# Optimization experiments

Measured on AMD Instinct MI355X. Metric: run time of the kernel, lower is better.

The kernel has to match this reference:

```python
import jax, jax.numpy as jnp
import numpy as np

N_NODES = 50000
N_EDGES = 800000
BASIS = 64
HIDDEN_RO = 128
N_GRAPHS = 512
T = 3


def setup_inputs() -> dict:
    key = jax.random.key(0)
    ks = jax.random.split(key, 12)
    Z = jax.random.randint(ks[0], (N_NODES,), 0, 10)
    edge_index = jax.random.randint(ks[1], (2, N_EDGES), 0, N_NODES)
    edge_attr = jax.random.normal(ks[2], (N_EDGES, BASIS), dtype=jnp.float32)
    batch = jnp.sort(jax.random.randint(ks[3], (N_NODES,), 0, N_GRAPHS))
    s = 1.0 / np.sqrt(BASIS)
    embed = jax.random.normal(ks[4], (10, BASIS), dtype=jnp.float32)
    cfW = jax.random.uniform(ks[5], (BASIS, BASIS), jnp.float32, -s, s)
    cfb = jax.random.uniform(ks[6], (BASIS,), jnp.float32, -s, s)
    dfW = jax.random.uniform(ks[7], (BASIS, BASIS), jnp.float32, -s, s)
    dfb = jax.random.uniform(ks[8], (BASIS,), jnp.float32, -s, s)
    fcW = jax.random.uniform(ks[9], (BASIS, BASIS), jnp.float32, -s, s)  # no bias
    W1 = jax.random.uniform(ks[10], (BASIS, HIDDEN_RO), jnp.float32, -s, s)
    b1 = jnp.zeros((HIDDEN_RO,), jnp.float32)
    W2 = jax.random.uniform(ks[11], (HIDDEN_RO, 4), jnp.float32, -1.0 / np.sqrt(HIDDEN_RO), 1.0 / np.sqrt(HIDDEN_RO))
    b2 = jnp.zeros((4,), jnp.float32)
    return {"Z": Z, "edge_index": edge_index, "edge_attr": edge_attr, "batch": batch,
            "embed": embed, "cfW": cfW, "cfb": cfb, "dfW": dfW, "dfb": dfb, "fcW": fcW,
            "W1": W1, "b1": b1, "W2": W2, "b2": b2}


def reference(Z, edge_index, edge_attr, batch, embed, cfW, cfb, dfW, dfb, fcW, W1, b1, W2, b2):
    src, dst = edge_index[0], edge_index[1]  # x_j gathered from src, aggregated at dst
    C = embed[Z]  # [N, basis]
    # df(edge_attr) does not depend on C; compute once (same math, shared weights)
    d_feat = edge_attr @ dfW + dfb  # [E, basis]
    for _ in range(T):
        c_feat = C[src] @ cfW + cfb            # gather + linear  [E, basis]
        msg = jnp.tanh((c_feat * d_feat) @ fcW)  # [E, basis]
        agg = jax.ops.segment_sum(msg, dst, num_segments=N_NODES)
        C = C + agg
    h = jnp.tanh(C @ W1 + b1) @ W2 + b2        # readout MLP [N, 4]
    return jax.ops.segment_sum(h, batch, num_segments=N_GRAPHS)  # global_add_pool [G, 4]
```

## Files before the change

kernel.cpp:

```cpp
#include <hip/hip_runtime.h>
#include <math.h>

#define N_NODES   50000
#define N_EDGES   800000
#define BASIS     64
#define HIDDEN_RO 128
#define N_GRAPHS  512
#define T_ITERS   3
#define NB_SCAN   ((N_NODES + 255) / 256)

typedef short s8 __attribute__((ext_vector_type(8)));
typedef float f4 __attribute__((ext_vector_type(4)));

#define MFMA16(a, b, c) __builtin_amdgcn_mfma_f32_16x16x32_bf16(a, b, c, 0, 0, 0)

__device__ __forceinline__ float fast_tanh(float x) {
    float e = __expf(2.0f * x);
    return 1.0f - 2.0f / (e + 1.0f);
}

__device__ __forceinline__ f4 splat4(float x) { f4 v; v[0]=x; v[1]=x; v[2]=x; v[3]=x; return v; }

__device__ __forceinline__ void split8(const float* x, s8& hi, s8& lo) {
    union { unsigned a[4]; s8 v; } H, L;
    #pragma unroll
    for (int j = 0; j < 4; ++j) {
        float e0 = x[2*j], e1 = x[2*j+1];
        unsigned u0 = __float_as_uint(e0), u1 = __float_as_uint(e1);
        H.a[j] = (u0 >> 16) | (u1 & 0xFFFF0000u);
        float l0 = e0 - __uint_as_float(u0 & 0xFFFF0000u);
        float l1 = e1 - __uint_as_float(u1 & 0xFFFF0000u);
        L.a[j] = (__float_as_uint(l0) >> 16) | (__float_as_uint(l1) & 0xFFFF0000u);
    }
    hi = H.v; lo = L.v;
}

__device__ __forceinline__ void packW_dev(const float* __restrict__ W, s8* __restrict__ img, int t) {
    int lane = t & 63, q = lane >> 4, c = lane & 15;
    int f0 = (t >> 6) * 2;
    #pragma unroll
    for (int f = f0; f < f0 + 2; ++f) {
        int ks = f >> 2, g = f & 3;
        float tv[8];
        #pragma unroll
        for (int j = 0; j < 8; ++j)
            tv[j] = W[(ks*32 + q*8 + j) * 64 + g*16 + c];
        s8 hi, lo;
        split8(tv, hi, lo);
        img[f * 64 + lane]       = hi;
        img[(8 + f) * 64 + lane] = lo;
    }
}

__device__ __forceinline__ void packW1_dev(const float* __restrict__ W, s8* __restrict__ img, int t) {
    int lane = t & 63, q = lane >> 4, c = lane & 15;
    int f0 = (t >> 6) * 4;
    #pragma unroll
    for (int f = f0; f < f0 + 4; ++f) {
        int ks = f >> 3, g = f & 7;
        float tv[8];
        #pragma unroll
        for (int j = 0; j < 8; ++j)
            tv[j] = W[(ks*32 + q*8 + j) * HIDDEN_RO + g*16 + c];
        s8 hi, lo;
        split8(tv, hi, lo);
        img[f * 64 + lane]        = hi;
        img[(16 + f) * 64 + lane] = lo;
    }
}

__global__ void k_packW(const float* __restrict__ W0, const float* __restrict__ W1m,
                        const float* __restrict__ W2m, const float* __restrict__ W1ro,
                        s8* __restrict__ i0, s8* __restrict__ i1, s8* __restrict__ i2,
                        s8* __restrict__ i3) {
    int b = blockIdx.x, t = threadIdx.x;
    if (b == 0) packW_dev(W0, i0, t);
    else if (b == 1) packW_dev(W1m, i1, t);
    else if (b == 2) packW_dev(W2m, i2, t);
    else packW1_dev(W1ro, i3, t);
}

__global__ void k_init_hist(const int* __restrict__ Z, const float* __restrict__ embed,
                            float* __restrict__ C, const int* __restrict__ dst,
                            int* __restrict__ deg) {
    int i = blockIdx.x * blockDim.x + threadIdx.x;
    if (i < N_NODES * BASIS) { int n = i >> 6, c = i & 63; C[i] = embed[Z[n] * 64 + c]; }
    if (i < N_EDGES) atomicAdd(&deg[dst[i]], 1);
}

__global__ void k_scan1(const int* __restrict__ deg, int* __restrict__ off,
                        int* __restrict__ bsum) {
    __shared__ int ws[4];
    int b = blockIdx.x, t = threadIdx.x, lane = t & 63, w = t >> 6;
    int i = b * 256 + t;
    int v = (i < N_NODES) ? deg[i] : 0;
    int s = v;
    #pragma unroll
    for (int ofs = 1; ofs < 64; ofs <<= 1) {
        int tmp = __shfl_up(s, ofs, 64);
        if (lane >= ofs) s += tmp;
    }
    if (lane == 63) ws[w] = s;
    __syncthreads();
    if (t == 0) {
        int a = 0;
        #pragma unroll
        for (int k = 0; k < 4; ++k) { int x = ws[k]; ws[k] = a; a += x; }
        bsum[b] = a;
    }
    __syncthreads();
    int excl = ws[w] + s - v;
    if (i < N_NODES) off[i] = excl;
}

__global__ void k_scan2(int* __restrict__ bsum) {
    __shared__ int ws[4];
    int t = threadIdx.x, lane = t & 63, w = t >> 6;
    int v = (t < NB_SCAN) ? bsum[t] : 0;
    int s = v;
    #pragma unroll
    for (int ofs = 1; ofs < 64; ofs <<= 1) {
        int tmp = __shfl_up(s, ofs, 64);
        if (lane >= ofs) s += tmp;
    }
    if (lane == 63) ws[w] = s;
    __syncthreads();
    if (t == 0) {
        int a = 0;
        #pragma unroll
        for (int k = 0; k < 4; ++k) { int x = ws[k]; ws[k] = a; a += x; }
    }
    __syncthreads();
    int excl = ws[w] + s - v;
    if (t < NB_SCAN) bsum[t] = excl;
}

__global__ void k_scan3(const int* __restrict__ deg, int* __restrict__ off,
                        const int* __restrict__ bsum, int* __restrict__ cursor) {
    int b = blockIdx.x, i = b * 256 + threadIdx.x;
    if (i < N_NODES) {
        int val = off[i] + bsum[b];
        off[i] = val;
        cursor[i] = val;
        if (i == N_NODES - 1) off[N_NODES] = val + deg[i];
    }
}

__global__ void k_fill(const int* __restrict__ src, const int* __restrict__ dst,
                       int* __restrict__ cursor, int* __restrict__ slot_s,
                       int* __restrict__ slot_p) {
    int e = blockIdx.x * blockDim.x + threadIdx.x;
    if (e < N_EDGES) {
        int d = dst[e], s = src[e];
        int p = atomicAdd(&cursor[d], 1);
        slot_s[p] = s;
        slot_p[e] = p;
    }
}

template <int MODE>
__global__ __launch_bounds__(256, 4) void k_gemm64L(const float* __restrict__ in,
        const s8* __restrict__ wimg, const float* __restrict__ b,
        const int* __restrict__ map, float* __restrict__ out, int rows) {
    __shared__ s8 LW[1024];
    int t = threadIdx.x;
    for (int i = t; i < 1024; i += 256) LW[i] = wimg[i];
    __syncthreads();
    int lane = t & 63, wv = t >> 6, q = lane >> 4, c = lane & 15;
    float bias[4];
    #pragma unroll
    for (int g = 0; g < 4; ++g) bias[g] = b[g*16 + c];
    int chunks = (rows + 15) >> 4;
    int wave = blockIdx.x * 4 + wv, nw = gridDim.x * 4;
    for (int ch = wave; ch < chunks; ch += nw) {
        int base = ch << 4;
        int row = base + c;
        bool valid = row < rows;
        int r = valid ? row : 0;
        const float4* ip = (const float4*)(in + (size_t)r * 64);
        s8 ahi[2], alo[2];
        #pragma unroll
        for (int ks = 0; ks < 2; ++ks) {
            float4 a0 = ip[ks*8 + q*2 + 0];
            float4 a1 = ip[ks*8 + q*2 + 1];
            float xs[8] = {a0.x,a0.y,a0.z,a0.w, a1.x,a1.y,a1.z,a1.w};
            if (!valid) {
                #pragma unroll
                for (int j = 0; j < 8; ++j) xs[j] = 0.0f;
            }
            split8(xs, ahi[ks], alo[ks]);
        }
        int orow[4];
        #pragma unroll
        for (int r2 = 0; r2 < 4; ++r2) {
            int ro = base + q*4 + r2;
            if (ro >= rows) ro = rows - 1;
            orow[r2] = (MODE == 2) ? map[ro] : ro;
        }
        f4 acc[4];
        #pragma unroll
        for (int g = 0; g < 4; ++g) acc[g] = splat4(bias[g]);
        #pragma unroll
        for (int ks = 0; ks < 2; ++ks)
            #pragma unroll
            for (int g = 0; g < 4; ++g) {
                s8 wh = LW[(ks*4 + g) * 64 + lane];
                s8 wl = LW[(8 + ks*4 + g) * 64 + lane];
                acc[g] = MFMA16(ahi[ks], wh, acc[g]);
                acc[g] = MFMA16(ahi[ks], wl, acc[g]);
                acc[g] = MFMA16(alo[ks], wh, acc[g]);
            }
        #pragma unroll
        for (int g = 0; g < 4; ++g)
            #pragma unroll
            for (int r2 = 0; r2 < 4; ++r2) {
                if (base + q*4 + r2 < rows)
                    out[(size_t)orow[r2] * 64 + g*16 + c] = acc[g][r2];
            }
    }
}

__global__ __launch_bounds__(256, 4) void k_mp5(const float* __restrict__ CF,
        const float* __restrict__ DF, const s8* __restrict__ wimg,
        const int* __restrict__ slot_s, const int* __restrict__ off,
        float* __restrict__ C) {
    __shared__ s8 LW[1024];
    int t = threadIdx.x;
    for (int i = t; i < 1024; i += 256) LW[i] = wimg[i];
    __syncthreads();
    int lane = t & 63, wv = t >> 6, q = lane >> 4, c = lane & 15;
    int wave = blockIdx.x * 4 + wv, nw = gridDim.x * 4;
    for (int n = wave; n < N_NODES; n += nw) {
        int beg = off[n], end = off[n + 1];
        if (beg >= end) continue;
        float acc0 = 0.f, acc1 = 0.f, acc2 = 0.f, acc3 = 0.f;
        int sl0 = beg + c; if (sl0 >= end) sl0 = end - 1;
        int srcn = slot_s[sl0];
        #pragma unroll 1
        for (int base = beg; base < end; base += 16) {
            int slot = base + c;
            bool valid = slot < end;
            if (!valid) slot = end - 1;
            int scur = srcn;
            if (base + 16 < end) {
                int s2 = base + 16 + c; if (s2 >= end) s2 = end - 1;
                srcn = slot_s[s2];
            }
            const float4* dp = (const float4*)(DF + (size_t)slot * 64);
            float4 d0 = dp[q*2],     d1 = dp[q*2 + 1];
            float4 d2 = dp[8 + q*2], d3 = dp[8 + q*2 + 1];
            const float4* cp = (const float4*)(CF + (size_t)scur * 64);
            float4 c0 = cp[q*2],     c1 = cp[q*2 + 1];
            float4 c2 = cp[8 + q*2], c3 = cp[8 + q*2 + 1];
            s8 ahi[2], alo[2];
            {
                float xs[8] = {c0.x*d0.x, c0.y*d0.y, c0.z*d0.z, c0.w*d0.w,
                               c1.x*d1.x, c1.y*d1.y, c1.z*d1.z, c1.w*d1.w};
                if (!valid) {
                    #pragma unroll
                    for (int j = 0; j < 8; ++j) xs[j] = 0.0f;
                }
                split8(xs, ahi[0], alo[0]);
                float ys[8] = {c2.x*d2.x, c2.y*d2.y, c2.z*d2.z, c2.w*d2.w,
                               c3.x*d3.x, c3.y*d3.y, c3.z*d3.z, c3.w*d3.w};
                if (!valid) {
                    #pragma unroll
                    for (int j = 0; j < 8; ++j) ys[j] = 0.0f;
                }
                split8(ys, ahi[1], alo[1]);
            }
            f4 d[4];
            #pragma unroll
            for (int g = 0; g < 4; ++g) d[g] = splat4(0.0f);
            #pragma unroll
            for (int ks = 0; ks < 2; ++ks)
                #pragma unroll
                for (int g = 0; g < 4; ++g) {
                    s8 wh = LW[(ks*4 + g) * 64 + lane];
                    s8 wl = LW[(8 + ks*4 + g) * 64 + lane];
                    d[g] = MFMA16(ahi[ks], wh, d[g]);
                    d[g] = MFMA16(ahi[ks], wl, d[g]);
                    d[g] = MFMA16(alo[ks], wh, d[g]);
                }
            acc0 += fast_tanh(d[0][0]) + fast_tanh(d[0][1]) + fast_tanh(d[0][2]) + fast_tanh(d[0][3]);
            acc1 += fast_tanh(d[1][0]) + fast_tanh(d[1][1]) + fast_tanh(d[1][2]) + fast_tanh(d[1][3]);
            acc2 += fast_tanh(d[2][0]) + fast_tanh(d[2][1]) + fast_tanh(d[2][2]) + fast_tanh(d[2][3]);
            acc3 += fast_tanh(d[3][0]) + fast_tanh(d[3][1]) + fast_tanh(d[3][2]) + fast_tanh(d[3][3]);
        }
        acc0 += __shfl_xor(acc0, 16, 64); acc0 += __shfl_xor(acc0, 32, 64);
        acc1 += __shfl_xor(acc1, 16, 64); acc1 += __shfl_xor(acc1, 32, 64);
        acc2 += __shfl_xor(acc2, 16, 64); acc2 += __shfl_xor(acc2, 32, 64);
        acc3 += __shfl_xor(acc3, 16, 64); acc3 += __shfl_xor(acc3, 32, 64);
        float v = (q == 0) ? acc0 : (q == 1) ? acc1 : (q == 2) ? acc2 : acc3;
        C[(size_t)n * 64 + lane] += v;
    }
}

__global__ __launch_bounds__(256) void k_gemm64_fb(const float* __restrict__ in,
        const float* __restrict__ W, const float* __restrict__ b,
        float* __restrict__ out, int rows) {
    int r = blockIdx.x * blockDim.x + threadIdx.x;
    if (r >= rows) return;
    float acc[BASIS];
    #pragma unroll
    for (int c = 0; c < BASIS; ++c) acc[c] = b[c];
    const float4* in4 = (const float4*)(in + (size_t)r * BASIS);
    #pragma unroll 1
    for (int k0 = 0; k0 < 16; ++k0) {
        float4 xv = in4[k0];
        #pragma unroll
        for (int c = 0; c < BASIS; ++c)
            acc[c] += xv.x * W[(4*k0+0)*64+c] + xv.y * W[(4*k0+1)*64+c]
                    + xv.z * W[(4*k0+2)*64+c] + xv.w * W[(4*k0+3)*64+c];
    }
    #pragma unroll
    for (int c = 0; c < BASIS; ++c) out[(size_t)r * BASIS + c] = acc[c];
}
__global__ __launch_bounds__(256) void k_edge_fb(const float* __restrict__ CF,
        const float* __restrict__ ea, const float* __restrict__ dfW,
        const float* __restrict__ dfb, const float* __restrict__ fcW,
        const int* __restrict__ src, const int* __restrict__ dst,
        float* __restrict__ C) {
    int e = blockIdx.x * blockDim.x + threadIdx.x;
    if (e >= N_EDGES) return;
    int s = src[e], d = dst[e];
    float dfeat[BASIS];
    #pragma unroll
    for (int c = 0; c < BASIS; ++c) dfeat[c] = dfb[c];
    const float4* ea4 = (const float4*)(ea + (size_t)e * BASIS);
    #pragma unroll
    for (int k0 = 0; k0 < 16; ++k0) {
        float4 xv = ea4[k0];
        #pragma unroll
        for (int c = 0; c < BASIS; ++c)
            dfeat[c] += xv.x * dfW[(4*k0+0)*64+c] + xv.y * dfW[(4*k0+1)*64+c]
                      + xv.z * dfW[(4*k0+2)*64+c] + xv.w * dfW[(4*k0+3)*64+c];
    }
    const float4* cf4 = (const float4*)(CF + (size_t)s * BASIS);
    float acc[BASIS];
    #pragma unroll
    for (int c = 0; c < BASIS; ++c) acc[c] = 0.0f;
    #pragma unroll
    for (int k0 = 0; k0 < 16; ++k0) {
        float4 a = cf4[k0];
        float x0 = a.x * dfeat[4*k0+0], x1 = a.y * dfeat[4*k0+1];
        float x2 = a.z * dfeat[4*k0+2], x3 = a.w * dfeat[4*k0+3];
        #pragma unroll
        for (int c = 0; c < BASIS; ++c)
            acc[c] += x0 * fcW[(4*k0+0)*64+c] + x1 * fcW[(4*k0+1)*64+c]
                    + x2 * fcW[(4*k0+2)*64+c] + x3 * fcW[(4*k0+3)*64+c];
    }
    float* crow = C + (size_t)d * BASIS;
    #pragma unroll
    for (int c = 0; c < BASIS; ++c) atomicAdd(&crow[c], fast_tanh(acc[c]));
}

__global__ __launch_bounds__(256) void k_readout2(const float* __restrict__ C,
        const float* __restrict__ W1, const float* __restrict__ b1,
        const float* __restrict__ W2, const float* __restrict__ b2,
        const int* __restrict__ batch, float* __restrict__ out) {
    __shared__ float w1[BASIS * HIDDEN_RO];
    __shared__ float xbuf[4][64];
    int t = threadIdx.x;
    for (int i = t; i < BASIS * HIDDEN_RO; i += 256) w1[i] = W1[i];
    __syncthreads();
    int lane = t & 63, wv = t >> 6;
    float b1a = b1[lane], b1b = b1[64 + lane];
    float4 w2a = ((const float4*)W2)[lane];
    float4 w2b = ((const float4*)W2)[64 + lane];
    int wave = blockIdx.x * 4 + wv;
    int nw   = gridDim.x * 4;
    for (int n = wave; n < N_NODES; n += nw) {
        float x = C[(size_t)n * 64 + lane];
        xbuf[wv][lane] = x;
        __builtin_amdgcn_wave_barrier();
        const float4* xb = (const float4*)xbuf[wv];
        float sa = b1a, sb = b1b;
        #pragma unroll
        for (int k4 = 0; k4 < 16; ++k4) {
            float4 xv = xb[k4];
            const float* r0 = &w1[(4*k4 + 0) * HIDDEN_RO];
            const float* r1 = &w1[(4*k4 + 1) * HIDDEN_RO];
            const float* r2 = &w1[(4*k4 + 2) * HIDDEN_RO];
            const float* r3 = &w1[(4*k4 + 3) * HIDDEN_RO];
            sa += xv.x * r0[lane]      + xv.y * r1[lane]
                + xv.z * r2[lane]      + xv.w * r3[lane];
            sb += xv.x * r0[64 + lane] + xv.y * r1[64 + lane]
                + xv.z * r2[64 + lane] + xv.w * r3[64 + lane];
        }
        float ha = fast_tanh(sa), hb = fast_tanh(sb);
        float v0 = ha * w2a.x + hb * w2b.x;
        float v1 = ha * w2a.y + hb * w2b.y;
        float v2 = ha * w2a.z + hb * w2b.z;
        float v3 = ha * w2a.w + hb * w2b.w;
        #pragma unroll
        for (int ofs = 32; ofs >= 1; ofs >>= 1) {
            v0 += __shfl_down(v0, ofs, 64);
            v1 += __shfl_down(v1, ofs, 64);
            v2 += __shfl_down(v2, ofs, 64);
            v3 += __shfl_down(v3, ofs, 64);
        }
        if (lane == 0) {
            int g = batch[n];
            atomicAdd(&out[(size_t)g * 4 + 0], v0);
            atomicAdd(&out[(size_t)g * 4 + 1], v1);
            atomicAdd(&out[(size_t)g * 4 + 2], v2);
            atomicAdd(&out[(size_t)g * 4 + 3], v3);
        }
        __builtin_amdgcn_wave_barrier();
    }
}

__global__ __launch_bounds__(256, 2) void k_readout3(const float* __restrict__ C,
        const s8* __restrict__ wimg, const float* __restrict__ b1,
        const float* __restrict__ W2, const float* __restrict__ b2,
        const int* __restrict__ batch, float* __restrict__ out) {
    __shared__ s8 LW[2048];
    int t = threadIdx.x;
    for (int i = t; i < 2048; i += 256) LW[i] = wimg[i];
    __syncthreads();
    int lane = t & 63, wv = t >> 6, q = lane >> 4, c = lane & 15;
    float bias[8];
    #pragma unroll
    for (int g = 0; g < 8; ++g) bias[g] = b1[g*16 + c];
    f4 w2r[8];
    #pragma unroll
    for (int g = 0; g < 8; ++g) {
        float4 w4 = ((const float4*)W2)[g*16 + c];
        w2r[g][0] = w4.x; w2r[g][1] = w4.y; w2r[g][2] = w4.z; w2r[g][3] = w4.w;
    }
    float4 b2v = *(const float4*)b2;
    int chunks = (N_NODES + 15) >> 4;
    int wave = blockIdx.x * 4 + wv, nw = gridDim.x * 4;
    for (int ch = wave; ch < chunks; ch += nw) {
        int base = ch << 4;
        int row = base + c;
        bool valid = row < N_NODES;
        int r = valid ? row : 0;
        const float4* ip = (const float4*)(C + (size_t)r * 64);
        s8 ahi[2], alo[2];
        #pragma unroll
        for (int ks = 0; ks < 2; ++ks) {
            float4 a0 = ip[ks*8 + q*2 + 0];
            float4 a1 = ip[ks*8 + q*2 + 1];
            float xs[8] = {a0.x,a0.y,a0.z,a0.w, a1.x,a1.y,a1.z,a1.w};
            if (!valid) {
                #pragma unroll
                for (int j = 0; j < 8; ++j) xs[j] = 0.0f;
            }
            split8(xs, ahi[ks], alo[ks]);
        }
        f4 acc[8];
        #pragma unroll
        for (int g = 0; g < 8; ++g) acc[g] = splat4(bias[g]);
        #pragma unroll
        for (int ks = 0; ks < 2; ++ks)
            #pragma unroll
            for (int g = 0; g < 8; ++g) {
                s8 wh = LW[(ks*8 + g) * 64 + lane];
                s8 wl = LW[(16 + ks*8 + g) * 64 + lane];
                acc[g] = MFMA16(ahi[ks], wh, acc[g]);
                acc[g] = MFMA16(ahi[ks], wl, acc[g]);
                acc[g] = MFMA16(alo[ks], wh, acc[g]);
            }
        f4 v4[4];
        #pragma unroll
        for (int r2 = 0; r2 < 4; ++r2) v4[r2] = splat4(0.0f);
        #pragma unroll
        for (int g = 0; g < 8; ++g)
            #pragma unroll
            for (int r2 = 0; r2 < 4; ++r2) {
                float h = fast_tanh(acc[g][r2]);
                #pragma unroll
                for (int j = 0; j < 4; ++j) v4[r2][j] += h * w2r[g][j];
            }
        #pragma unroll
        for (int r2 = 0; r2 < 4; ++r2)
            #pragma unroll
            for (int j = 0; j < 4; ++j) {
                float x = v4[r2][j];
                x += __shfl_xor(x, 1, 64);
                x += __shfl_xor(x, 2, 64);
                x += __shfl_xor(x, 4, 64);
                x += __shfl_xor(x, 8, 64);
                v4[r2][j] = x;
            }
        if (c == 0) {
            #pragma unroll
            for (int r2 = 0; r2 < 4; ++r2) {
                int ro = base + q*4 + r2;
                if (ro < N_NODES) {
                    int g_id = batch[ro];
                    atomicAdd(&out[(size_t)g_id * 4 + 0], v4[r2][0] + b2v.x);
                    atomicAdd(&out[(size_t)g_id * 4 + 1], v4[r2][1] + b2v.y);
                    atomicAdd(&out[(size_t)g_id * 4 + 2], v4[r2][2] + b2v.z);
                    atomicAdd(&out[(size_t)g_id * 4 + 3], v4[r2][3] + b2v.w);
                }
            }
        }
    }
}

extern "C" void kernel_launch(void* const* d_in, const int* in_sizes, int n_in,
                              void* d_out, int out_size, void* d_ws, size_t ws_size,
                              hipStream_t stream) {
    const int*   Z     = (const int*)d_in[0];
    const int*   ei    = (const int*)d_in[1];
    const float* ea    = (const float*)d_in[2];
    const int*   batch = (const int*)d_in[3];
    const float* embed = (const float*)d_in[4];
    const float* cfW   = (const float*)d_in[5];
    const float* cfb   = (const float*)d_in[6];
    const float* dfW   = (const float*)d_in[7];
    const float* dfb   = (const float*)d_in[8];
    const float* fcW   = (const float*)d_in[9];
    const float* W1    = (const float*)d_in[10];
    const float* b1    = (const float*)d_in[11];
    const float* W2    = (const float*)d_in[12];
    const float* b2    = (const float*)d_in[13];
    const int* src = ei;
    const int* dst = ei + N_EDGES;
    float* out = (float*)d_out;

    const size_t bC = (size_t)N_NODES * BASIS * sizeof(float);
    const size_t bE = (size_t)N_EDGES * sizeof(int);
    const size_t bO = (size_t)(N_NODES + 1) * sizeof(int);
    const size_t bI = 1024 * sizeof(s8);
    char* p = (char*)d_ws;
    float* C      = (float*)p;  p += bC;
    float* CF     = (float*)p;  p += bC;
    int*   slotP  = (int*)p;    p += bE;
    int*   slotS  = (int*)p;    p += bE;
    int*   deg    = (int*)p;    p += bO;
    int*   off    = (int*)p;    p += bO;
    int*   cursor = (int*)p;    p += bO;
    p = (char*)(((uintptr_t)p + 255) & ~(uintptr_t)255);
    s8* imgDF = (s8*)p;  p += bI;
    s8* imgCF = (s8*)p;  p += bI;
    s8* imgFC = (s8*)p;  p += bI;
    s8* imgW1 = (s8*)p;  p += 2048 * sizeof(s8);
    int* bsum = (int*)p; p += 256 * sizeof(int);
    float* DF = (float*)p;
    const size_t need = (size_t)(p - (char*)d_ws) + (size_t)N_EDGES * BASIS * sizeof(float);
    const bool full = ws_size >= need;

    hipMemsetAsync(d_out, 0, (size_t)out_size * sizeof(float), stream);

    if (full) {
        hipMemsetAsync(deg, 0, bO, stream);
        k_init_hist<<<(N_NODES * BASIS + 255) / 256, 256, 0, stream>>>(Z, embed, C, dst, deg);
        k_packW<<<4, 256, 0, stream>>>(dfW, cfW, fcW, W1, imgDF, imgCF, imgFC, imgW1);
        k_scan1<<<NB_SCAN, 256, 0, stream>>>(deg, off, bsum);
        k_scan2<<<1, 256, 0, stream>>>(bsum);
        k_scan3<<<NB_SCAN, 256, 0, stream>>>(deg, off, bsum, cursor);
        k_fill<<<(N_EDGES + 255) / 256, 256, 0, stream>>>(src, dst, cursor, slotS, slotP);
        k_gemm64L<2><<<4096, 256, 0, stream>>>(ea, imgDF, dfb, slotP, DF, N_EDGES);
        for (int t = 0; t < T_ITERS; ++t) {
            k_gemm64L<0><<<800, 256, 0, stream>>>(C, imgCF, cfb, nullptr, CF, N_NODES);
            k_mp5<<<2048, 256, 0, stream>>>(CF, DF, imgFC, slotS, off, C);
        }
        k_readout3<<<1024, 256, 0, stream>>>(C, imgW1, b1, W2, b2, batch, out);
    } else {
        k_init_hist<<<(N_NODES * BASIS + 255) / 256, 256, 0, stream>>>(Z, embed, C, dst, (int*)CF);
        for (int t = 0; t < T_ITERS; ++t) {
            k_gemm64_fb<<<(N_NODES + 255) / 256, 256, 0, stream>>>(C, cfW, cfb, CF, N_NODES);
            k_edge_fb<<<(N_EDGES + 255) / 256, 256, 0, stream>>>(CF, ea, dfW, dfb, fcW, src, dst, C);
        }
        k_readout2<<<512, 256, 0, stream>>>(C, W1, b1, W2, b2, batch, out);
    }
}
```

Baseline: 869.9 us.

## Switch message passing from node-per-wave to edge-chunk scheduling with segmented atomics

The message-passing kernel now walks fixed 16-edge chunks of the dst-sorted edge list instead of one destination node per wave. Each slot packs dst and src into one 32-bit word (16 bits each) so a wave can find segment boundaries inside the chunk. It then reduces each run of equal destinations and adds it to C with atomicAdd. This removes the padding waste and load imbalance from low-degree nodes and drops the offset lookups, at the cost of atomics. The packing assumes node ids fit in 16 bits, but N_NODES is 50000, which fits only because that is under 65536. It also assumes N_EDGES is a multiple of 16.

After: 805.8 us. -7.4%, faster.

```diff
diff --git a/kernel.cpp b/kernel.cpp
--- a/kernel.cpp
+++ b/kernel.cpp
@@ -147,13 +147,13 @@
 }
 
 __global__ void k_fill(const int* __restrict__ src, const int* __restrict__ dst,
-                       int* __restrict__ cursor, int* __restrict__ slot_s,
+                       int* __restrict__ cursor, unsigned* __restrict__ slot_sn,
                        int* __restrict__ slot_p) {
     int e = blockIdx.x * blockDim.x + threadIdx.x;
     if (e < N_EDGES) {
         int d = dst[e], s = src[e];
         int p = atomicAdd(&cursor[d], 1);
-        slot_s[p] = s;
+        slot_sn[p] = ((unsigned)d << 16) | (unsigned)s;
         slot_p[e] = p;
     }
 }
@@ -220,79 +220,78 @@
     }
 }
 
-__global__ __launch_bounds__(256, 4) void k_mp5(const float* __restrict__ CF,
+__global__ __launch_bounds__(256, 4) void k_mp8(const float* __restrict__ CF,
         const float* __restrict__ DF, const s8* __restrict__ wimg,
-        const int* __restrict__ slot_s, const int* __restrict__ off,
-        float* __restrict__ C) {
+        const unsigned* __restrict__ slot_sn, float* __restrict__ C) {
     __shared__ s8 LW[1024];
     int t = threadIdx.x;
     for (int i = t; i < 1024; i += 256) LW[i] = wimg[i];
     __syncthreads();
     int lane = t & 63, wv = t >> 6, q = lane >> 4, c = lane & 15;
     int wave = blockIdx.x * 4 + wv, nw = gridDim.x * 4;
-    for (int n = wave; n < N_NODES; n += nw) {
-        int beg = off[n], end = off[n + 1];
-        if (beg >= end) continue;
-        float acc0 = 0.f, acc1 = 0.f, acc2 = 0.f, acc3 = 0.f;
-        int sl0 = beg + c; if (sl0 >= end) sl0 = end - 1;
-        int srcn = slot_s[sl0];
-        #pragma unroll 1
-        for (int base = beg; base < end; base += 16) {
-            int slot = base + c;
-            bool valid = slot < end;
-            if (!valid) slot = end - 1;
-            int scur = srcn;
-            if (base + 16 < end) {
-                int s2 = base + 16 + c; if (s2 >= end) s2 = end - 1;
-                srcn = slot_s[s2];
-            }
-            const float4* dp = (const float4*)(DF + (size_t)slot * 64);
-            float4 d0 = dp[q*2],     d1 = dp[q*2 + 1];
-            float4 d2 = dp[8 + q*2], d3 = dp[8 + q*2 + 1];
-            const float4* cp = (const float4*)(CF + (size_t)scur * 64);
-            float4 c0 = cp[q*2],     c1 = cp[q*2 + 1];
-            float4 c2 = cp[8 + q*2], c3 = cp[8 + q*2 + 1];
-            s8 ahi[2], alo[2];
-            {
-                float xs[8] = {c0.x*d0.x, c0.y*d0.y, c0.z*d0.z, c0.w*d0.w,
-                               c1.x*d1.x, c1.y*d1.y, c1.z*d1.z, c1.w*d1.w};
-                if (!valid) {
-                    #pragma unroll
-                    for (int j = 0; j < 8; ++j) xs[j] = 0.0f;
-                }
-                split8(xs, ahi[0], alo[0]);
-                float ys[8] = {c2.x*d2.x, c2.y*d2.y, c2.z*d2.z, c2.w*d2.w,
-                               c3.x*d3.x, c3.y*d3.y, c3.z*d3.z, c3.w*d3.w};
-                if (!valid) {
-                    #pragma unroll
-                    for (int j = 0; j < 8; ++j) ys[j] = 0.0f;
-                }
-                split8(ys, ahi[1], alo[1]);
-            }
-            f4 d[4];
-            #pragma unroll
-            for (int g = 0; g < 4; ++g) d[g] = splat4(0.0f);
-            #pragma unroll
-            for (int ks = 0; ks < 2; ++ks)
-                #pragma unroll
-                for (int g = 0; g < 4; ++g) {
-                    s8 wh = LW[(ks*4 + g) * 64 + lane];
-                    s8 wl = LW[(8 + ks*4 + g) * 64 + lane];
-                    d[g] = MFMA16(ahi[ks], wh, d[g]);
-                    d[g] = MFMA16(ahi[ks], wl, d[g]);
-                    d[g] = MFMA16(alo[ks], wh, d[g]);
-                }
-            acc0 += fast_tanh(d[0][0]) + fast_tanh(d[0][1]) + fast_tanh(d[0][2]) + fast_tanh(d[0][3]);
-            acc1 += fast_tanh(d[1][0]) + fast_tanh(d[1][1]) + fast_tanh(d[1][2]) + fast_tanh(d[1][3]);
-            acc2 += fast_tanh(d[2][0]) + fast_tanh(d[2][1]) + fast_tanh(d[2][2]) + fast_tanh(d[2][3]);
-            acc3 += fast_tanh(d[3][0]) + fast_tanh(d[3][1]) + fast_tanh(d[3][2]) + fast_tanh(d[3][3]);
-        }
-        acc0 += __shfl_xor(acc0, 16, 64); acc0 += __shfl_xor(acc0, 32, 64);
-        acc1 += __shfl_xor(acc1, 16, 64); acc1 += __shfl_xor(acc1, 32, 64);
-        acc2 += __shfl_xor(acc2, 16, 64); acc2 += __shfl_xor(acc2, 32, 64);
-        acc3 += __shfl_xor(acc3, 16, 64); acc3 += __shfl_xor(acc3, 32, 64);
-        float v = (q == 0) ? acc0 : (q == 1) ? acc1 : (q == 2) ? acc2 : acc3;
-        C[(size_t)n * 64 + lane] += v;
+    const int NCH = N_EDGES >> 4;
+    for (int ch = wave; ch < NCH; ch += nw) {
+        int slot = (ch << 4) + c;
+        unsigned sn = slot_sn[slot];
+        int sA  = (int)(sn & 0xFFFFu);
+        int myn = (int)(sn >> 16);
+        const float4* dp = (const float4*)(DF + (size_t)slot * 64);
+        float4 d0 = dp[q*2],     d1 = dp[q*2 + 1];
+        float4 d2 = dp[8 + q*2], d3 = dp[8 + q*2 + 1];
+        const float4* cp = (const float4*)(CF + (size_t)sA * 64);
+        float4 c0 = cp[q*2],     c1 = cp[q*2 + 1];
+        float4 c2 = cp[8 + q*2], c3 = cp[8 + q*2 + 1];
+        s8 ahi[2], alo[2];
+        {
+            float xs[8] = {c0.x*d0.x, c0.y*d0.y, c0.z*d0.z, c0.w*d0.w,
+                           c1.x*d1.x, c1.y*d1.y, c1.z*d1.z, c1.w*d1.w};
+            split8(xs, ahi[0], alo[0]);
+            float ys[8] = {c2.x*d2.x, c2.y*d2.y, c2.z*d2.z, c2.w*d2.w,
+                           c3.x*d3.x, c3.y*d3.y, c3.z*d3.z, c3.w*d3.w};
+            split8(ys, ahi[1], alo[1]);
+        }
+        f4 d[4];
+        #pragma unroll
+        for (int g = 0; g < 4; ++g) d[g] = splat4(0.0f);
+        #pragma unroll
+        for (int ks = 0; ks < 2; ++ks)
+            #pragma unroll
+            for (int g = 0; g < 4; ++g) {
+                s8 wh = LW[(ks*4 + g) * 64 + lane];
+                s8 wl = LW[(8 + ks*4 + g) * 64 + lane];
+                d[g] = MFMA16(ahi[ks], wh, d[g]);
+                d[g] = MFMA16(ahi[ks], wl, d[g]);
+                d[g] = MFMA16(alo[ks], wh, d[g]);
+            }
+        #pragma unroll
+        for (int g = 0; g < 4; ++g)
+            #pragma unroll
+            for (int r2 = 0; r2 < 4; ++r2)
+                d[g][r2] = fast_tanh(d[g][r2]);
+        int nrow[4];
+        #pragma unroll
+        for (int r2 = 0; r2 < 4; ++r2) nrow[r2] = __shfl(myn, q*4 + r2, 64);
+        int segN = __shfl(myn, 0, 64);
+        while (true) {
+            float s0 = 0.f, s1 = 0.f, s2 = 0.f, s3 = 0.f;
+            #pragma unroll
+            for (int r2 = 0; r2 < 4; ++r2) {
+                bool in = (nrow[r2] == segN);
+                s0 += in ? d[0][r2] : 0.0f;
+                s1 += in ? d[1][r2] : 0.0f;
+                s2 += in ? d[2][r2] : 0.0f;
+                s3 += in ? d[3][r2] : 0.0f;
+            }
+            s0 += __shfl_xor(s0, 16, 64); s0 += __shfl_xor(s0, 32, 64);
+            s1 += __shfl_xor(s1, 16, 64); s1 += __shfl_xor(s1, 32, 64);
+            s2 += __shfl_xor(s2, 16, 64); s2 += __shfl_xor(s2, 32, 64);
+            s3 += __shfl_xor(s3, 16, 64); s3 += __shfl_xor(s3, 32, 64);
+            float v = (q == 0) ? s0 : (q == 1) ? s1 : (q == 2) ? s2 : s3;
+            atomicAdd(&C[(size_t)segN * 64 + lane], v);
+            unsigned long long m = __ballot((lane < 16) && (myn > segN));
+            if (m == 0ull) break;
+            segN = __shfl(myn, __ffsll((unsigned long long)m) - 1, 64);
+        }
     }
 }
 
@@ -530,7 +529,7 @@
     float* C      = (float*)p;  p += bC;
     float* CF     = (float*)p;  p += bC;
     int*   slotP  = (int*)p;    p += bE;
-    int*   slotS  = (int*)p;    p += bE;
+    unsigned* slotSN = (unsigned*)p; p += bE;
     int*   deg    = (int*)p;    p += bO;
     int*   off    = (int*)p;    p += bO;
     int*   cursor = (int*)p;    p += bO;
@@ -553,11 +552,11 @@
         k_scan1<<<NB_SCAN, 256, 0, stream>>>(deg, off, bsum);
         k_scan2<<<1, 256, 0, stream>>>(bsum);
         k_scan3<<<NB_SCAN, 256, 0, stream>>>(deg, off, bsum, cursor);
-        k_fill<<<(N_EDGES + 255) / 256, 256, 0, stream>>>(src, dst, cursor, slotS, slotP);
+        k_fill<<<(N_EDGES + 255) / 256, 256, 0, stream>>>(src, dst, cursor, slotSN, slotP);
         k_gemm64L<2><<<4096, 256, 0, stream>>>(ea, imgDF, dfb, slotP, DF, N_EDGES);
         for (int t = 0; t < T_ITERS; ++t) {
             k_gemm64L<0><<<800, 256, 0, stream>>>(C, imgCF, cfb, nullptr, CF, N_NODES);
-            k_mp5<<<2048, 256, 0, stream>>>(CF, DF, imgFC, slotS, off, C);
+            k_mp8<<<2048, 256, 0, stream>>>(CF, DF, imgFC, slotSN, C);
         }
         k_readout3<<<1024, 256, 0, stream>>>(C, imgW1, b1, W2, b2, batch, out);
     } else {
```
